# Optimization experiments

Hardware: AMD Instinct MI355X
Metric: run time of the kernel (lower is better)

Reference implementation:

```python
import jax, jax.numpy as jnp
import numpy as np

# --- constants from the module (KANLayer passes degree=3; BSplineActivation defaults) ---
K = 5          # num_control_points
DEG = 3        # degree
G = 3          # grid points (set_grid_points(3) in __init__)
LO, HI = -1.0, 1.0  # grid_range


def basis_table():
    """Precompute the shared [G, K] normalized Gaussian basis table (same for all edges)."""
    knots = np.linspace(LO - DEG * 0.1, HI + DEG * 0.1, K + DEG + 1)
    grid = np.linspace(LO, HI, G)
    bv = np.zeros((G, K), dtype=np.float32)
    for i in range(K):
        center = (knots[i + DEG // 2] + knots[i + DEG // 2 + 1]) / 2.0
        width = (knots[i + DEG + 1] - knots[i]) / 2.0
        bv[:, i] = np.exp(-(((grid - center) / width) ** 2))
    bv = bv / (bv.sum(axis=1, keepdims=True) + 1e-6)
    return jnp.asarray(bv)


def kan_layer(x, cp, bw, sw, imp, bv):
    """Fused KANLayer: x [B,I]; cp [I,J,K]; bw/sw/imp [I,J]; bv [G,K] -> [B,J]."""
    xc = jnp.clip(x, LO, HI)
    gi = (xc - LO) / (HI - LO) * (G - 1)                     # [B,I] in [0, G-1]
    lo = jnp.clip(jnp.floor(gi).astype(jnp.int32), 0, G - 1)
    hi = jnp.clip(jnp.ceil(gi).astype(jnp.int32), 0, G - 1)
    frac = (gi - lo.astype(gi.dtype))[..., None]             # [B,I,1]
    basis = bv[lo] * (1.0 - frac) + bv[hi] * frac            # [B,I,K] gather + lerp
    base = x * jax.nn.sigmoid(x)                             # SiLU base function, [B,I]
    # out[b,j] = sum_i imp[i,j] * (bw[i,j]*base[b,i] + sw[i,j]*basis[b,i,:]@cp[i,j,:])
    out = jnp.einsum('bi,ij->bj', base, imp * bw)
    out = out + jnp.einsum('bik,ijk->bj', basis, imp[:, :, None] * sw[:, :, None] * cp)
    return out


def setup_inputs() -> dict:
    key = jax.random.key(0)
    ks = jax.random.split(key, 9)
    B, D0, D1, D2 = 131072, 64, 128, 64
    return {
        'x': jax.random.normal(ks[0], (B, D0), dtype=jnp.float32),
        'cp0': jax.random.normal(ks[1], (D0, D1, K), dtype=jnp.float32) * 0.1,
        'bw0': jax.random.normal(ks[2], (D0, D1), dtype=jnp.float32),
        'sw0': jax.random.normal(ks[3], (D0, D1), dtype=jnp.float32),
        'imp0': jnp.ones((D0, D1), dtype=jnp.float32),
        'cp1': jax.random.normal(ks[4], (D1, D2, K), dtype=jnp.float32) * 0.1,
        'bw1': jax.random.normal(ks[5], (D1, D2), dtype=jnp.float32),
        'sw1': jax.random.normal(ks[6], (D1, D2), dtype=jnp.float32),
        'imp1': jnp.ones((D1, D2), dtype=jnp.float32),
    }


def reference(x, cp0, bw0, sw0, imp0, cp1, bw1, sw1, imp1):
    bv = basis_table()
    h = kan_layer(x, cp0, bw0, sw0, imp0, bv)
    return kan_layer(h, cp1, bw1, sw1, imp1, bv)
```

## Files before the change

### kernel.cpp

```cpp
#include <hip/hip_runtime.h>
#include <math.h>

typedef __attribute__((ext_vector_type(8))) _Float16 f16x8;
typedef __attribute__((ext_vector_type(2))) _Float16 f16x2;
typedef __attribute__((ext_vector_type(4))) float f32x4;


#define TPB 256
#define BM  128
#define HSTRIDE 272
#define W_OFF   34816
#define LDS_TOT (34816 + 16384)

#if __has_builtin(__builtin_amdgcn_global_load_lds)
#define HAVE_GLL 1
typedef const __attribute__((address_space(1))) unsigned int glb_u32;
typedef __attribute__((address_space(3))) unsigned int lds_u32;
#else
#define HAVE_GLL 0
#endif

__global__ __launch_bounds__(TPB, 3) void kan_mfma_kernel(
    const float* __restrict__ x, const _Float16* __restrict__ W0t,
    const _Float16* __restrict__ W1t, const float* __restrict__ bias0,
    const float* __restrict__ bias1, float* __restrict__ out)
{
    __shared__ char smem[LDS_TOT];
    const int tid  = threadIdx.x;
    const int lane = tid & 63;
    const int wid  = tid >> 6;
    const int gq   = lane >> 4;
    const int lm   = lane & 15;
    const int wavebase = wid * 32;
    const long rowbase = (long)blockIdx.x * BM;

    auto stageChunk = [&](const char* gsrc_chunk, int bufoff) {
#if HAVE_GLL
        const char* gs = gsrc_chunk + wid * 2048 + lane * 16;
        char* ls = smem + W_OFF + bufoff + wid * 2048;
        __builtin_amdgcn_global_load_lds((glb_u32*)gs, (lds_u32*)ls, 16, 0, 0);
        __builtin_amdgcn_global_load_lds((glb_u32*)(gs + 1024), (lds_u32*)(ls + 1024), 16, 0, 0);
#else
        float4 a = *(const float4*)(gsrc_chunk + tid * 32);
        float4 b = *(const float4*)(gsrc_chunk + tid * 32 + 16);
        *(float4*)(smem + W_OFF + bufoff + tid * 32)      = a;
        *(float4*)(smem + W_OFF + bufoff + tid * 32 + 16) = b;
#endif
    };

#if __has_builtin(__builtin_amdgcn_cvt_pkrtz)
    auto pk2 = [](float a, float b) -> f16x2 {
        return (f16x2)__builtin_amdgcn_cvt_pkrtz(a, b);
    };
#else
    auto pk2 = [](float a, float b) -> f16x2 {
        return f16x2{(_Float16)a, (_Float16)b};
    };
#endif
#if __has_builtin(__builtin_amdgcn_rcpf)
    auto frcp = [](float a) -> float { return __builtin_amdgcn_rcpf(a); };
#else
    auto frcp = [](float a) -> float { return 1.0f / a; };
#endif

    auto buildFeats4 = [&](const float* v, f16x8* dst) {
        union U { f16x8 v8; f16x2 h2[4]; } u0, u1, u2, u3;
        #pragma unroll
        for (int q = 0; q < 4; ++q) {
            float va = v[2 * q], vb = v[2 * q + 1];
            float ba = va * frcp(1.0f + __expf(-va));
            float bb = vb * frcp(1.0f + __expf(-vb));
            float ga = fminf(fmaxf(va, -1.f), 1.f) + 1.f;
            float gb = fminf(fmaxf(vb, -1.f), 1.f) + 1.f;
            float s1a = (ga >= 1.f) ? 1.f : 0.f;
            float s1b = (gb >= 1.f) ? 1.f : 0.f;
            float sga = (ga >= 1.f) ? ga : 0.f;
            float sgb = (gb >= 1.f) ? gb : 0.f;
            u0.h2[q] = pk2(ba, bb);
            u1.h2[q] = pk2(ga, gb);
            u2.h2[q] = pk2(s1a, s1b);
            u3.h2[q] = pk2(sga, sgb);
        }
        dst[0] = u0.v8; dst[1] = u1.v8; dst[2] = u2.v8; dst[3] = u3.v8;
    };

    float b0v[8], b1v[4];
    #pragma unroll
    for (int nf = 0; nf < 8; ++nf) b0v[nf] = bias0[nf * 16 + lm];
    #pragma unroll
    for (int nf = 0; nf < 4; ++nf) b1v[nf] = bias1[nf * 16 + lm];

    float v0[2][8], v1[2][8];
    #pragma unroll
    for (int mi = 0; mi < 2; ++mi) {
        const float* xp = x + (rowbase + wavebase + mi * 16 + lm) * 64 + gq * 8;
        float4 a0 = *(const float4*)(xp);
        float4 a1 = *(const float4*)(xp + 4);
        float4 a2 = *(const float4*)(xp + 32);
        float4 a3 = *(const float4*)(xp + 36);
        v0[mi][0]=a0.x; v0[mi][1]=a0.y; v0[mi][2]=a0.z; v0[mi][3]=a0.w;
        v0[mi][4]=a1.x; v0[mi][5]=a1.y; v0[mi][6]=a1.z; v0[mi][7]=a1.w;
        v1[mi][0]=a2.x; v1[mi][1]=a2.y; v1[mi][2]=a2.z; v1[mi][3]=a2.w;
        v1[mi][4]=a3.x; v1[mi][5]=a3.y; v1[mi][6]=a3.z; v1[mi][7]=a3.w;
    }

    f32x4 acc[2][8] = {};
    {
        const char* w0 = (const char*)W0t;
        const int lb0 = (gq * 128 + lm) * 16;

        stageChunk(w0, 0);
        f16x8 fr[2][4];
        buildFeats4(v0[0], fr[0]);
        buildFeats4(v0[1], fr[1]);
        __syncthreads();

#define L0_STEP(S, C) do {                                                    \
        if ((S) < 7)                                                          \
            stageChunk(w0 + ((S) + 1) * 8192, (((S) + 1) & 1) * 8192);        \
        const char* wb = smem + W_OFF + ((S) & 1) * 8192;                     \
        f16x8 bt[8];                                                          \
        _Pragma("unroll")                                                     \
        for (int nf = 0; nf < 8; ++nf)                                        \
            bt[nf] = *(const f16x8*)(wb + lb0 + nf * 256);                    \
        _Pragma("unroll")                                                     \
        for (int mi = 0; mi < 2; ++mi) {                                      \
            f16x8 a = fr[mi][C];                                              \
            _Pragma("unroll")                                                 \
            for (int nf = 0; nf < 8; ++nf)                                    \
                acc[mi][nf] = __builtin_amdgcn_mfma_f32_16x16x32_f16(         \
                    a, bt[nf], acc[mi][nf], 0, 0, 0);                         \
        }                                                                     \
        __syncthreads();                                                      \
    } while (0)

        L0_STEP(0, 0); L0_STEP(1, 1); L0_STEP(2, 2); L0_STEP(3, 3);
        buildFeats4(v1[0], fr[0]);
        buildFeats4(v1[1], fr[1]);
        L0_STEP(4, 0); L0_STEP(5, 1); L0_STEP(6, 2); L0_STEP(7, 3);
#undef L0_STEP
    }

    {
        #pragma unroll
        for (int mi = 0; mi < 2; ++mi)
            #pragma unroll
            for (int nf = 0; nf < 8; ++nf)
                #pragma unroll
                for (int rg = 0; rg < 4; ++rg)
                    *(_Float16*)(smem + (wavebase + mi * 16 + gq * 4 + rg) * HSTRIDE
                                 + (nf * 16 + lm) * 2) = (_Float16)(acc[mi][nf][rg] + b0v[nf]);
        __syncthreads();
        stageChunk((const char*)W1t, 0);
        __syncthreads();
    }

    f32x4 accO[2][4] = {};
    {
        const char* w1 = (const char*)W1t;
        const int lb1 = (gq * 64 + lm) * 16;
        f16x8 fr[2][4];

#define L1_SUB(BUFOFF, C) do {                                                \
        const char* wb = smem + W_OFF + (BUFOFF);                             \
        f16x8 bt[4];                                                          \
        _Pragma("unroll")                                                     \
        for (int nf = 0; nf < 4; ++nf)                                        \
            bt[nf] = *(const f16x8*)(wb + lb1 + nf * 256);                    \
        _Pragma("unroll")                                                     \
        for (int mi = 0; mi < 2; ++mi) {                                      \
            f16x8 a = fr[mi][C];                                              \
            _Pragma("unroll")                                                 \
            for (int nf = 0; nf < 4; ++nf)                                    \
                accO[mi][nf] = __builtin_amdgcn_mfma_f32_16x16x32_f16(        \
                    a, bt[nf], accO[mi][nf], 0, 0, 0);                        \
        }                                                                     \
    } while (0)

#define L1_STAGE(SG, C0, C1) do {                                            \
        if ((SG) < 7)                                                         \
            stageChunk(w1 + ((SG) + 1) * 8192, (((SG) + 1) & 1) * 8192);      \
        L1_SUB(((SG) & 1) * 8192, C0);                                        \
        L1_SUB(((SG) & 1) * 8192 + 4096, C1);                                 \
        __syncthreads();                                                      \
    } while (0)

#define L1_FEATS(HALF, IH) do {                                               \
        _Pragma("unroll")                                                     \
        for (int mi = 0; mi < 2; ++mi) {                                      \
            const char* hrow = smem + (wavebase + mi * 16 + lm) * HSTRIDE;    \
            f16x8 hv = *(const f16x8*)(hrow + ((HALF) * 64 + (IH) * 32 + gq * 8) * 2); \
            float v[8];                                                       \
            _Pragma("unroll")                                                 \
            for (int e = 0; e < 8; ++e) v[e] = (float)hv[e];                  \
            buildFeats4(v, fr[mi]);                                           \
        }                                                                     \
    } while (0)

        L1_FEATS(0, 0);
        L1_STAGE(0, 0, 1); L1_STAGE(1, 2, 3);
        L1_FEATS(0, 1);
        L1_STAGE(2, 0, 1); L1_STAGE(3, 2, 3);
        L1_FEATS(1, 0);
        L1_STAGE(4, 0, 1); L1_STAGE(5, 2, 3);
        L1_FEATS(1, 1);
        L1_STAGE(6, 0, 1); L1_STAGE(7, 2, 3);
#undef L1_SUB
#undef L1_STAGE
#undef L1_FEATS
    }

    float* og = out + (rowbase + wavebase) * 64;
    #pragma unroll
    for (int mi = 0; mi < 2; ++mi)
        #pragma unroll
        for (int nf = 0; nf < 4; ++nf)
            #pragma unroll
            for (int rg = 0; rg < 4; ++rg)
                og[(mi * 16 + gq * 4 + rg) * 64 + nf * 16 + lm] = accO[mi][nf][rg] + b1v[nf];
}

__global__ __launch_bounds__(256) void kan_combine_w(
    const float* __restrict__ cp0, const float* __restrict__ bw0,
    const float* __restrict__ sw0, const float* __restrict__ imp0,
    const float* __restrict__ cp1, const float* __restrict__ bw1,
    const float* __restrict__ sw1, const float* __restrict__ imp1,
    _Float16* __restrict__ W0t, _Float16* __restrict__ W1t,
    float* __restrict__ bias0, float* __restrict__ bias1)
{
    float bvv[3][5];
    #pragma unroll
    for (int g = 0; g < 3; ++g) {
        float gv = (float)g - 1.0f;
        float e[5]; float s = 0.f;
        #pragma unroll
        for (int i = 0; i < 5; ++i) {
            float cc = -0.8125f + 0.325f * (float)i;
            float d  = (gv - cc) * (1.0f / 0.65f);
            e[i] = __expf(-d * d); s += e[i];
        }
        float inv = 1.0f / (s + 1e-6f);
        #pragma unroll
        for (int i = 0; i < 5; ++i) bvv[g][i] = e[i] * inv;
    }

    auto wval = [&](const float* cp, float bw, float sw, float imp, int q) -> float {
        if (q == 0) return imp * bw;
        float P0 = 0.f, Q0 = 0.f, P1 = 0.f, Q1 = 0.f;
        #pragma unroll
        for (int c = 0; c < 5; ++c) {
            P0 += cp[c] * bvv[0][c];
            Q0 += cp[c] * (bvv[1][c] - bvv[0][c]);
            P1 += cp[c] * (2.f * bvv[1][c] - bvv[2][c]);
            Q1 += cp[c] * (bvv[2][c] - bvv[1][c]);
        }
        float r = (q == 1) ? Q0 : (q == 2) ? (P1 - P0) : (Q1 - Q0);
        return imp * sw * r;
    };
    auto p0val = [&](const float* cp) -> float {
        float P0 = 0.f;
        #pragma unroll
        for (int c = 0; c < 5; ++c) P0 += cp[c] * bvv[0][c];
        return P0;
    };

    const int bx = blockIdx.x;
    const int t  = threadIdx.x;

    if (bx < 256) {
        int f = bx * 256 + t;
        if (f < 32768) {
            int e = f & 7, n = (f >> 3) & 127, g = (f >> 10) & 3, s = f >> 12;
            int ih = s >> 2, q = s & 3;
            int i = ih * 32 + g * 8 + e;
            int edge = i * 128 + n;
            W0t[f] = (_Float16)wval(cp0 + edge * 5, bw0[edge], sw0[edge], imp0[edge], q);
        } else {
            int f2 = f - 32768;
            int e = f2 & 7, n = (f2 >> 3) & 63, g = (f2 >> 9) & 3;
            int tq = f2 >> 11;
            int half = tq >> 3, s = tq & 7;
            int ih = s >> 2, q = s & 3;
            int i2 = half * 64 + ih * 32 + g * 8 + e;
            int edge = i2 * 64 + n;
            W1t[f2] = (_Float16)wval(cp1 + edge * 5, bw1[edge], sw1[edge], imp1[edge], q);
        }
    } else if (bx < 272) {
        __shared__ float part[256];
        int bb = bx - 256;
        int jj = t >> 5, split = t & 31;
        int j = bb * 8 + jj;
        float s = 0.f;
        #pragma unroll
        for (int k = 0; k < 2; ++k) {
            int i = split * 2 + k;
            int edge = i * 128 + j;
            s += imp0[edge] * sw0[edge] * p0val(cp0 + edge * 5);
        }
        part[t] = s;
        __syncthreads();
        if (t < 8) {
            float acc = 0.f;
            #pragma unroll
            for (int k = 0; k < 32; ++k) acc += part[t * 32 + k];
            bias0[bb * 8 + t] = acc;
        }
    } else {
        __shared__ float part[256];
        int bb = bx - 272;
        int jj = t >> 6, split = t & 63;
        int j = bb * 4 + jj;
        float s = 0.f;
        #pragma unroll
        for (int k = 0; k < 2; ++k) {
            int i2 = split * 2 + k;
            int edge = i2 * 64 + j;
            s += imp1[edge] * sw1[edge] * p0val(cp1 + edge * 5);
        }
        part[t] = s;
        __syncthreads();
        if (t < 4) {
            float acc = 0.f;
            #pragma unroll
            for (int k = 0; k < 64; ++k) acc += part[t * 64 + k];
            bias1[bb * 4 + t] = acc;
        }
    }
}

#define NTHR 256
#define JT 32
#define WS8 8

#define STAGE_L0(JBASE) do {                                                  \
    _Pragma("unroll")                                                         \
    for (int p = 0; p < 8; ++p) {                                             \
        int idx = tid + p * NTHR;                                             \
        int i  = idx >> 5;                                                    \
        int jj = idx & 31;                                                    \
        int e  = i * 128 + (JBASE) + jj;                                      \
        float im = imp0[e];                                                   \
        float wb = bw0[e] * im;                                               \
        float ws = sw0[e] * im;                                               \
        const float* cp = cp0 + e * 5;                                        \
        float* wp = wbuf + idx * WS8;                                         \
        wp[0] = wb;                                                           \
        wp[1] = ws * cp[0]; wp[2] = ws * cp[1]; wp[3] = ws * cp[2];           \
        wp[4] = ws * cp[3]; wp[5] = ws * cp[4];                               \
    }                                                                         \
} while (0)

#define STAGE_L1(IBASE, JBASE) do {                                           \
    _Pragma("unroll")                                                         \
    for (int p = 0; p < 8; ++p) {                                             \
        int idx = tid + p * NTHR;                                             \
        int ii = idx >> 5;                                                    \
        int jj = idx & 31;                                                    \
        int e  = ((IBASE) + ii) * 64 + (JBASE) + jj;                          \
        float im = imp1[e];                                                   \
        float wb = bw1[e] * im;                                               \
        float ws = sw1[e] * im;                                               \
        const float* cp = cp1 + e * 5;                                        \
        float* wp = wbuf + idx * WS8;                                         \
        wp[0] = wb;                                                           \
        wp[1] = ws * cp[0]; wp[2] = ws * cp[1]; wp[3] = ws * cp[2];           \
        wp[4] = ws * cp[3]; wp[5] = ws * cp[4];                               \
    }                                                                         \
} while (0)

#define COMPUTE_TILE(ACC) do {                                                \
    _Pragma("unroll 2")                                                       \
    for (int i = 0; i < 64; ++i) {                                            \
        float v  = vbuf[i][tid];                                              \
        float sg = 1.0f / (1.0f + __expf(-v));                                \
        float base = v * sg;                                                  \
        float xc = fminf(fmaxf(v, -1.0f), 1.0f);                              \
        float gi = xc + 1.0f;                                                 \
        int lo = (int)gi; lo = (lo > 2) ? 2 : lo;                             \
        float fr = gi - (float)lo;                                            \
        int hi = (fr > 0.0f) ? (lo + 1) : lo;                                 \
        float b0 = bvt[lo][0]; b0 += (bvt[hi][0] - b0) * fr;                  \
        float b1 = bvt[lo][1]; b1 += (bvt[hi][1] - b1) * fr;                  \
        float b2 = bvt[lo][2]; b2 += (bvt[hi][2] - b2) * fr;                  \
        float b3 = bvt[lo][3]; b3 += (bvt[hi][3] - b3) * fr;                  \
        float b4 = bvt[lo][4]; b4 += (bvt[hi][4] - b4) * fr;                  \
        const float* wr = wbuf + i * (JT * WS8);                              \
        _Pragma("unroll")                                                     \
        for (int jj = 0; jj < JT; ++jj) {                                     \
            const float* wp = wr + jj * WS8;                                  \
            float a = ACC[jj];                                                \
            a = fmaf(wp[0], base, a);                                         \
            a = fmaf(wp[1], b0, a);                                           \
            a = fmaf(wp[2], b1, a);                                           \
            a = fmaf(wp[3], b2, a);                                           \
            a = fmaf(wp[4], b3, a);                                           \
            a = fmaf(wp[5], b4, a);                                           \
            ACC[jj] = a;                                                      \
        }                                                                     \
    }                                                                         \
} while (0)

__global__ __launch_bounds__(NTHR) void kan_fused_kernel(
    const float* __restrict__ x,
    const float* __restrict__ cp0, const float* __restrict__ bw0,
    const float* __restrict__ sw0, const float* __restrict__ imp0,
    const float* __restrict__ cp1, const float* __restrict__ bw1,
    const float* __restrict__ sw1, const float* __restrict__ imp1,
    float* __restrict__ out)
{
    __shared__ float vbuf[64][NTHR + 1];
    __shared__ float wbuf[64 * JT * WS8];
    __shared__ float bvt[3][8];

    const int tid = threadIdx.x;

    if (tid < 3) {
        float gv = -1.0f + (float)tid;
        float e[5];
        float s = 0.0f;
        #pragma unroll
        for (int i = 0; i < 5; ++i) {
            float c = -0.8125f + 0.325f * (float)i;
            float d = (gv - c) * (1.0f / 0.65f);
            e[i] = expf(-d * d);
            s += e[i];
        }
        float inv = 1.0f / (s + 1e-6f);
        #pragma unroll
        for (int i = 0; i < 5; ++i) bvt[tid][i] = e[i] * inv;
    }

    {
        const float4* xg = (const float4*)(x + (size_t)blockIdx.x * (NTHR * 64));
        #pragma unroll
        for (int it = 0; it < 16; ++it) {
            int e4 = tid + it * NTHR;
            float4 v = xg[e4];
            int r  = e4 >> 4;
            int ib = (e4 & 15) << 2;
            vbuf[ib + 0][r] = v.x;
            vbuf[ib + 1][r] = v.y;
            vbuf[ib + 2][r] = v.z;
            vbuf[ib + 3][r] = v.w;
        }
    }
    __syncthreads();

    float h0[32] = {}, h1[32] = {}, h2[32] = {}, h3[32] = {};
    STAGE_L0(0);   __syncthreads(); COMPUTE_TILE(h0); __syncthreads();
    STAGE_L0(32);  __syncthreads(); COMPUTE_TILE(h1); __syncthreads();
    STAGE_L0(64);  __syncthreads(); COMPUTE_TILE(h2); __syncthreads();
    STAGE_L0(96);  __syncthreads(); COMPUTE_TILE(h3); __syncthreads();

    #pragma unroll
    for (int i = 0; i < 32; ++i) vbuf[i][tid] = h0[i];
    #pragma unroll
    for (int i = 0; i < 32; ++i) vbuf[32 + i][tid] = h1[i];

    float o0[32] = {}, o1[32] = {};
    STAGE_L1(0, 0);   __syncthreads(); COMPUTE_TILE(o0); __syncthreads();
    STAGE_L1(0, 32);  __syncthreads(); COMPUTE_TILE(o1); __syncthreads();

    #pragma unroll
    for (int i = 0; i < 32; ++i) vbuf[i][tid] = h2[i];
    #pragma unroll
    for (int i = 0; i < 32; ++i) vbuf[32 + i][tid] = h3[i];

    STAGE_L1(64, 0);  __syncthreads(); COMPUTE_TILE(o0); __syncthreads();
    STAGE_L1(64, 32); __syncthreads(); COMPUTE_TILE(o1);

    float4* og = (float4*)(out + (size_t)blockIdx.x * (NTHR * 64) + (size_t)tid * 64);
    #pragma unroll
    for (int q = 0; q < 8; ++q)
        og[q] = make_float4(o0[4 * q + 0], o0[4 * q + 1], o0[4 * q + 2], o0[4 * q + 3]);
    #pragma unroll
    for (int q = 0; q < 8; ++q)
        og[8 + q] = make_float4(o1[4 * q + 0], o1[4 * q + 1], o1[4 * q + 2], o1[4 * q + 3]);
}

extern "C" void kernel_launch(void* const* d_in, const int* in_sizes, int n_in,
                              void* d_out, int out_size, void* d_ws, size_t ws_size,
                              hipStream_t stream) {
    const float* x    = (const float*)d_in[0];
    const float* cp0  = (const float*)d_in[1];
    const float* bw0  = (const float*)d_in[2];
    const float* sw0  = (const float*)d_in[3];
    const float* imp0 = (const float*)d_in[4];
    const float* cp1  = (const float*)d_in[5];
    const float* bw1  = (const float*)d_in[6];
    const float* sw1  = (const float*)d_in[7];
    const float* imp1 = (const float*)d_in[8];
    float* out = (float*)d_out;

    const int B = in_sizes[0] / 64;
    const size_t need = 65536 * sizeof(_Float16) + 192 * sizeof(float);

    if (ws_size >= need && (B % BM) == 0) {
        _Float16* W0t = (_Float16*)d_ws;
        _Float16* W1t = W0t + 32768;
        float* bias0 = (float*)(W1t + 32768);
        float* bias1 = bias0 + 128;
        kan_combine_w<<<288, 256, 0, stream>>>(cp0, bw0, sw0, imp0,
                                               cp1, bw1, sw1, imp1,
                                               W0t, W1t, bias0, bias1);
        kan_mfma_kernel<<<B / BM, TPB, 0, stream>>>(x, W0t, W1t, bias0, bias1, out);
    } else {
        kan_fused_kernel<<<B / NTHR, NTHR, 0, stream>>>(
            x, cp0, bw0, sw0, imp0, cp1, bw1, sw1, imp1, out);
    }
}
```

Baseline: 37.43 us.

## Deepen weight staging to a four-buffer ring with vmcnt-based waits

Replaces the double-buffered weight staging with a four-slot LDS ring that prefetches three chunks ahead. Full __syncthreads are swapped for explicit s_waitcnt vmcnt counts plus raw s_barrier, so loads stay in flight across steps. The extra LDS grows the footprint, so launch bounds drop from 3 to 2 blocks per CU and occupancy falls. Register pins keep the x and bias values live. The vmcnt counts are hand-tuned and depend on how many loads are outstanding, which risks races if the compiler reorders or adds memory ops.

```diff
diff --git a/kernel.cpp b/kernel.cpp
--- a/kernel.cpp
+++ b/kernel.cpp
@@ -10,7 +10,7 @@
 #define BM  128
 #define HSTRIDE 272
 #define W_OFF   34816
-#define LDS_TOT (34816 + 16384)
+#define LDS_TOT (34816 + 4 * 8192)
 
 #if __has_builtin(__builtin_amdgcn_global_load_lds)
 #define HAVE_GLL 1
@@ -20,7 +20,15 @@
 #define HAVE_GLL 0
 #endif
 
-__global__ __launch_bounds__(TPB, 3) void kan_mfma_kernel(
+#if HAVE_GLL
+#define WAIT_DMA(N) asm volatile("s_waitcnt vmcnt(" #N ")" ::: "memory")
+#else
+#define WAIT_DMA(N) asm volatile("s_waitcnt vmcnt(0) lgkmcnt(0)" ::: "memory")
+#endif
+#define BAR() __builtin_amdgcn_s_barrier()
+#define PIN(f) asm volatile("" : "+v"(f))
+
+__global__ __launch_bounds__(TPB, 2) void kan_mfma_kernel(
     const float* __restrict__ x, const _Float16* __restrict__ W0t,
     const _Float16* __restrict__ W1t, const float* __restrict__ bias0,
     const float* __restrict__ bias1, float* __restrict__ out)
@@ -103,22 +111,31 @@
         v1[mi][0]=a2.x; v1[mi][1]=a2.y; v1[mi][2]=a2.z; v1[mi][3]=a2.w;
         v1[mi][4]=a3.x; v1[mi][5]=a3.y; v1[mi][6]=a3.z; v1[mi][7]=a3.w;
     }
+    #pragma unroll
+    for (int mi = 0; mi < 2; ++mi)
+        #pragma unroll
+        for (int e = 0; e < 8; ++e) { PIN(v0[mi][e]); PIN(v1[mi][e]); }
+    #pragma unroll
+    for (int nf = 0; nf < 8; ++nf) PIN(b0v[nf]);
+    #pragma unroll
+    for (int nf = 0; nf < 4; ++nf) PIN(b1v[nf]);
 
     f32x4 acc[2][8] = {};
+    f16x8 fr[2][4];
     {
         const char* w0 = (const char*)W0t;
         const int lb0 = (gq * 128 + lm) * 16;
 
-        stageChunk(w0, 0);
-        f16x8 fr[2][4];
+        stageChunk(w0 + 0 * 8192, 0 * 8192);
+        stageChunk(w0 + 1 * 8192, 1 * 8192);
+        stageChunk(w0 + 2 * 8192, 2 * 8192);
         buildFeats4(v0[0], fr[0]);
         buildFeats4(v0[1], fr[1]);
-        __syncthreads();
-
-#define L0_STEP(S, C) do {                                                    \
-        if ((S) < 7)                                                          \
-            stageChunk(w0 + ((S) + 1) * 8192, (((S) + 1) & 1) * 8192);        \
-        const char* wb = smem + W_OFF + ((S) & 1) * 8192;                     \
+        WAIT_DMA(4);
+        BAR();
+
+#define L0_STEP(S, C, VN) do {                                                \
+        const char* wb = smem + W_OFF + ((S) % 4) * 8192;                     \
         f16x8 bt[8];                                                          \
         _Pragma("unroll")                                                     \
         for (int nf = 0; nf < 8; ++nf)                                        \
@@ -131,17 +148,22 @@
                 acc[mi][nf] = __builtin_amdgcn_mfma_f32_16x16x32_f16(         \
                     a, bt[nf], acc[mi][nf], 0, 0, 0);                         \
         }                                                                     \
-        __syncthreads();                                                      \
+        if ((S) < 5)                                                          \
+            stageChunk(w0 + ((S) + 3) * 8192, (((S) + 3) % 4) * 8192);        \
+        if ((S) < 7) { WAIT_DMA(VN); BAR(); }                                 \
     } while (0)
 
-        L0_STEP(0, 0); L0_STEP(1, 1); L0_STEP(2, 2); L0_STEP(3, 3);
+        L0_STEP(0, 0, 4); L0_STEP(1, 1, 4);
+        L0_STEP(2, 2, 4); L0_STEP(3, 3, 4);
         buildFeats4(v1[0], fr[0]);
         buildFeats4(v1[1], fr[1]);
-        L0_STEP(4, 0); L0_STEP(5, 1); L0_STEP(6, 2); L0_STEP(7, 3);
+        L0_STEP(4, 0, 4); L0_STEP(5, 1, 2);
+        L0_STEP(6, 2, 0); L0_STEP(7, 3, 0);
 #undef L0_STEP
     }
 
     {
+        const char* w1 = (const char*)W1t;
         #pragma unroll
         for (int mi = 0; mi < 2; ++mi)
             #pragma unroll
@@ -150,16 +172,17 @@
                 for (int rg = 0; rg < 4; ++rg)
                     *(_Float16*)(smem + (wavebase + mi * 16 + gq * 4 + rg) * HSTRIDE
                                  + (nf * 16 + lm) * 2) = (_Float16)(acc[mi][nf][rg] + b0v[nf]);
-        __syncthreads();
-        stageChunk((const char*)W1t, 0);
-        __syncthreads();
+        stageChunk(w1 + 0 * 8192, 0 * 8192);
+        stageChunk(w1 + 1 * 8192, 1 * 8192);
+        stageChunk(w1 + 2 * 8192, 2 * 8192);
+        WAIT_DMA(4);
+        BAR();
     }
 
     f32x4 accO[2][4] = {};
     {
         const char* w1 = (const char*)W1t;
         const int lb1 = (gq * 64 + lm) * 16;
-        f16x8 fr[2][4];
 
 #define L1_SUB(BUFOFF, C) do {                                                \
         const char* wb = smem + W_OFF + (BUFOFF);                             \
@@ -177,12 +200,12 @@
         }                                                                     \
     } while (0)
 
-#define L1_STAGE(SG, C0, C1) do {                                            \
-        if ((SG) < 7)                                                         \
-            stageChunk(w1 + ((SG) + 1) * 8192, (((SG) + 1) & 1) * 8192);      \
-        L1_SUB(((SG) & 1) * 8192, C0);                                        \
-        L1_SUB(((SG) & 1) * 8192 + 4096, C1);                                 \
-        __syncthreads();                                                      \
+#define L1_STEP(SG, C0, C1, VN) do {                                          \
+        L1_SUB(((SG) % 4) * 8192, C0);                                        \
+        L1_SUB(((SG) % 4) * 8192 + 4096, C1);                                 \
+        if ((SG) < 5)                                                         \
+            stageChunk(w1 + ((SG) + 3) * 8192, (((SG) + 3) % 4) * 8192);      \
+        if ((SG) < 7) { WAIT_DMA(VN); BAR(); }                                \
     } while (0)
 
 #define L1_FEATS(HALF, IH) do {                                               \
@@ -198,15 +221,15 @@
     } while (0)
 
         L1_FEATS(0, 0);
-        L1_STAGE(0, 0, 1); L1_STAGE(1, 2, 3);
+        L1_STEP(0, 0, 1, 4); L1_STEP(1, 2, 3, 4);
         L1_FEATS(0, 1);
-        L1_STAGE(2, 0, 1); L1_STAGE(3, 2, 3);
+        L1_STEP(2, 0, 1, 4); L1_STEP(3, 2, 3, 4);
         L1_FEATS(1, 0);
-        L1_STAGE(4, 0, 1); L1_STAGE(5, 2, 3);
+        L1_STEP(4, 0, 1, 4); L1_STEP(5, 2, 3, 2);
         L1_FEATS(1, 1);
-        L1_STAGE(6, 0, 1); L1_STAGE(7, 2, 3);
+        L1_STEP(6, 0, 1, 0); L1_STEP(7, 2, 3, 0);
 #undef L1_SUB
-#undef L1_STAGE
+#undef L1_STEP
 #undef L1_FEATS
     }
 
```

New measurement: 37.88 us. No clear change (+1.2%).
